# Performance work log

Measured on AMD Instinct MI355X. Metric: run time of the kernel, lower is better.

Reference implementation:

```python
import jax, jax.numpy as jnp
import numpy as np
import math

B, S, MEM, D, H = 2, 2048, 512, 1024, 16
DH = D // H  # 64


def setup_inputs() -> dict:
    key = jax.random.key(0)
    ks = jax.random.split(key, 12)
    s = 1.0 / math.sqrt(D)
    return {
        "x": jax.random.normal(ks[0], (B, S, D), jnp.float32),
        "mems": jax.random.normal(ks[1], (B, MEM, D), jnp.float32),
        "freqs_cis": jax.random.normal(ks[2], (S, 32), jnp.float32),
        "mask": jax.random.randint(ks[3], (B, MEM + S), 0, 2, jnp.int32),
        "Wq": jax.random.normal(ks[4], (D, D), jnp.float32) * s,
        "bq": jnp.zeros((D,), jnp.float32),
        "Wk": jax.random.normal(ks[5], (D, D), jnp.float32) * s,
        "bk": jnp.zeros((D,), jnp.float32),
        "Wv": jax.random.normal(ks[6], (D, D), jnp.float32) * s,
        "bv": jnp.zeros((D,), jnp.float32),
        "Wo": jax.random.normal(ks[7], (D, D), jnp.float32) * s,
        "bo": jnp.zeros((D,), jnp.float32),
    }


def _split_heads(t):
    # [B, T, D] -> [B, H, T, DH]
    b, t_, _ = t.shape
    return t.reshape(b, t_, H, DH).transpose(0, 2, 1, 3)


def reference(x, mems, freqs_cis, mask, Wq, bq, Wk, bk, Wv, bv, Wo, bo):
    # mems prepended along sequence for K/V (torch: c = cat([mems, x], 1))
    c = jnp.concatenate([mems, x], axis=1)  # [B, MEM+S, D]
    Q = _split_heads(x @ Wq.T + bq)          # [B, H, S, DH]
    K = _split_heads(c @ Wk.T + bk)          # [B, H, Skv, DH]
    V = _split_heads(c @ Wv.T + bv)          # [B, H, Skv, DH]

    scores = jnp.einsum("bhqd,bhkd->bhqk", Q, K) / math.sqrt(DH)
    m = mask.astype(jnp.float32)             # [B, Skv]
    scores = scores - 1e6 * (1.0 - m[:, None, None, :])
    attn = jax.nn.softmax(scores, axis=-1)   # dropout omitted (eval mode)
    out = jnp.einsum("bhqk,bhkd->bhqd", attn, V)  # [B, H, S, DH]
    out = out.transpose(0, 2, 1, 3).reshape(B, S, D)
    return out @ Wo.T + bo
```

## Files before the change

kernel.cpp:

```cpp
#include <hip/hip_runtime.h>
#include <math.h>

#define NB   2
#define SQ   2048
#define SMEM 512
#define SKVN 2560
#define ND   1024
#define NH   16
#define DHN  64
#define NBH  32

typedef unsigned short u16;
typedef short bf16x8 __attribute__((ext_vector_type(8)));
typedef float f32x4 __attribute__((ext_vector_type(4)));
typedef u16 u16x4 __attribute__((ext_vector_type(4)));
typedef u16 u16x8 __attribute__((ext_vector_type(8)));

#define CSC   0.1803368801111204f

__device__ __forceinline__ u16 f2bf(float f) {
    unsigned u = __float_as_uint(f);
    u += 0x7FFFu + ((u >> 16) & 1u);
    return (u16)(u >> 16);
}

__device__ __forceinline__ float bf2f(u16 v) {
    return __uint_as_float(((unsigned)v) << 16);
}

__device__ __forceinline__ void async16(u16* lds, const u16* g) {
    __builtin_amdgcn_global_load_lds(
        (const __attribute__((address_space(1))) void*)g,
        (__attribute__((address_space(3))) void*)lds, 16, 0, 0);
}

__device__ __forceinline__ unsigned lds_off(const void* p) {
    return (unsigned)(uintptr_t)(const __attribute__((address_space(3))) void*)p;
}

__device__ __forceinline__ u16x4 tr_read(unsigned a) {
    u16x4 d;
    asm volatile("ds_read_b64_tr_b16 %0, %1" : "=v"(d) : "v"(a) : "memory");
    return d;
}

__device__ __forceinline__ unsigned cvtpk(float lo, float hi) {
    unsigned r;
    asm("v_cvt_pk_bf16_f32 %0, %1, %2" : "=v"(r) : "v"(lo), "v"(hi));
    return r;
}

__device__ __forceinline__ float exp2r(float x) {
    float r;
    asm("v_exp_f32 %0, %1" : "=v"(r) : "v"(x));
    return r;
}

union PKU { unsigned u[2]; u16x4 v; };
union U8  { struct { u16x4 lo, hi; } p; bf16x8 v; };

__global__ __launch_bounds__(256)
void cvt_all(const float* __restrict__ x, const float* __restrict__ mems,
             const float* __restrict__ W0, const float* __restrict__ W1,
             const float* __restrict__ W2, const float* __restrict__ W3,
             u16* __restrict__ xb, u16* __restrict__ memb,
             u16* __restrict__ d0, u16* __restrict__ d1,
             u16* __restrict__ d2, u16* __restrict__ d3,
             const int* __restrict__ mask, u16* __restrict__ mb16)
{
    const int bid = blockIdx.x;
    if (bid >= 4608) {
        const int i = (bid - 4608) * 256 + threadIdx.x;
        if (i < NB * SKVN)
            mb16[i] = mask[i] ? (u16)0 : f2bf(1.0e6f * CSC);
        return;
    }
    size_t i = ((size_t)bid * 256 + threadIdx.x) * 8;
    const float* s; u16* d;
    if (i < 4194304) { s = x; d = xb; }
    else if (i < 5242880) { s = mems; d = memb; i -= 4194304; }
    else {
        size_t off = i - 5242880;
        const int wi = (int)(off >> 20);
        i = off & 1048575;
        switch (wi) {
            case 0:  s = W0; d = d0; break;
            case 1:  s = W1; d = d1; break;
            case 2:  s = W2; d = d2; break;
            default: s = W3; d = d3; break;
        }
    }
    float4 a = *(const float4*)(s + i);
    float4 b = *(const float4*)(s + i + 4);
    u16x8 o;
    o[0]=f2bf(a.x); o[1]=f2bf(a.y); o[2]=f2bf(a.z); o[3]=f2bf(a.w);
    o[4]=f2bf(b.x); o[5]=f2bf(b.y); o[6]=f2bf(b.z); o[7]=f2bf(b.w);
    *(u16x8*)(d + i) = o;
}

__device__ __forceinline__ const u16* arow_ptr(const u16* x, const u16* mems,
                                               int grow, int T, int memLen) {
    int b = grow >= T ? 1 : 0;
    int t = grow - b * T;
    if (memLen > 0 && t < memLen)
        return mems + ((size_t)(b * memLen + t)) * ND;
    return x + ((size_t)(b * (T - memLen) + (t - memLen))) * ND;
}

__device__ __forceinline__
void gemm64_body(const u16* __restrict__ x, const u16* __restrict__ mems,
                 const u16* __restrict__ W, const float* __restrict__ bias,
                 void* __restrict__ out, int T, int memLen, int mode,
                 int bx, int by, u16* As0, u16* As1, u16* Bs0, u16* Bs1)
{
    u16* As[2] = {As0, As1};
    u16* Bs[2] = {Bs0, Bs1};

    const int lane = threadIdx.x;
    const int lg = lane >> 4, li = lane & 15;
    const int row0 = bx * 64, col0 = by * 64;

    const int srow = lane >> 2;
    const int sslot = lane & 3;

    f32x4 acc[4][4];
    const f32x4 zf = {0.f, 0.f, 0.f, 0.f};
#pragma unroll
    for (int m = 0; m < 4; ++m)
#pragma unroll
        for (int n = 0; n < 4; ++n) acc[m][n] = zf;

    auto stage = [&](int c, int kt) {
        const int k0 = kt * 32;
#pragma unroll
        for (int ch = 0; ch < 4; ++ch) {
            const int r = ch * 16 + srow;
            const int gs = sslot ^ ((r ^ (r >> 2)) & 3);
            async16(&As[c][ch * 512],
                    arow_ptr(x, mems, row0 + r, T, memLen) + k0 + gs * 8);
        }
#pragma unroll
        for (int ch = 0; ch < 4; ++ch) {
            const int r = ch * 16 + srow;
            const int gs = sslot ^ ((r ^ (r >> 2)) & 3);
            async16(&Bs[c][ch * 512],
                    W + (size_t)(col0 + r) * ND + k0 + gs * 8);
        }
    };

    stage(0, 0);
    __builtin_amdgcn_sched_barrier(0);
    stage(1, 1);
    __builtin_amdgcn_sched_barrier(0);

    int cur = 0;
    for (int kt = 0; kt < 32; ++kt) {
        if (kt == 31) asm volatile("s_waitcnt vmcnt(0)" ::: "memory");
        else          asm volatile("s_waitcnt vmcnt(8)" ::: "memory");
        __builtin_amdgcn_sched_barrier(0);

        bf16x8 af[4], bfr[4];
#pragma unroll
        for (int m = 0; m < 4; ++m) {
            const int r = m * 16 + li;
            af[m] = *(const bf16x8*)&As[cur][r * 32 + ((lg ^ ((r ^ (r >> 2)) & 3)) << 3)];
        }
#pragma unroll
        for (int n = 0; n < 4; ++n) {
            const int r = n * 16 + li;
            bfr[n] = *(const bf16x8*)&Bs[cur][r * 32 + ((lg ^ ((r ^ (r >> 2)) & 3)) << 3)];
        }
        asm volatile("s_waitcnt lgkmcnt(0)" ::: "memory");
        __builtin_amdgcn_sched_barrier(0);
        if (kt + 2 < 32) stage(cur, kt + 2);

#pragma unroll
        for (int m = 0; m < 4; ++m)
#pragma unroll
            for (int n = 0; n < 4; ++n)
                acc[m][n] = __builtin_amdgcn_mfma_f32_16x16x32_bf16(
                                af[m], bfr[n], acc[m][n], 0, 0, 0);
        cur ^= 1;
    }

#pragma unroll
    for (int n = 0; n < 4; ++n) {
        const int col = col0 + n * 16 + li;
        const float bv = bias[col];
#pragma unroll
        for (int m = 0; m < 4; ++m) {
            const int rbase = row0 + m * 16 + 4 * lg;
            if (mode == 0) {
                float* o = (float*)out;
#pragma unroll
                for (int r = 0; r < 4; ++r)
                    o[(size_t)(rbase + r) * ND + col] = acc[m][n][r] + bv;
            } else if (mode == 1) {
                u16* o = (u16*)out;
                const int h = col >> 6, dh = col & 63;
#pragma unroll
                for (int r = 0; r < 4; ++r) {
                    const int grow = rbase + r;
                    const int b = grow >= T ? 1 : 0;
                    const int t = grow - b * T;
                    o[(((size_t)b * NH + h) * T + t) * DHN + dh] =
                        f2bf(acc[m][n][r] + bv);
                }
            } else {
                u16* o = (u16*)out;
                const int h = col >> 6, dh = col & 63;
                const int b = rbase >= T ? 1 : 0;
                const int t = rbase - b * T;
                u16x4 pk;
                pk[0] = f2bf(acc[m][n][0] + bv);
                pk[1] = f2bf(acc[m][n][1] + bv);
                pk[2] = f2bf(acc[m][n][2] + bv);
                pk[3] = f2bf(acc[m][n][3] + bv);
                *(u16x4*)&o[(((size_t)b * NH + h) * DHN + dh) * (size_t)T + t] = pk;
            }
        }
    }
}

__global__ __launch_bounds__(64)
void gemm_qkv(const u16* __restrict__ xb, const u16* __restrict__ memb,
              const u16* __restrict__ Wq, const float* __restrict__ bq, u16* Qb,
              const u16* __restrict__ Wk, const float* __restrict__ bk, u16* Kb,
              const u16* __restrict__ Wv, const float* __restrict__ bv, u16* Vtb)
{
    __shared__ u16 As[2][64 * 32];
    __shared__ u16 Bs[2][64 * 32];
    const int id = (blockIdx.x & 7) * 448 + (blockIdx.x >> 3);
    if (id < 1024) {
        gemm64_body(xb, nullptr, Wq, bq, Qb, SQ, 0, 1, id >> 4, id & 15,
                    As[0], As[1], Bs[0], Bs[1]);
    } else if (id < 2304) {
        const int t = id - 1024;
        gemm64_body(xb, memb, Wk, bk, Kb, SKVN, SMEM, 1, t >> 4, t & 15,
                    As[0], As[1], Bs[0], Bs[1]);
    } else {
        const int t = id - 2304;
        gemm64_body(xb, memb, Wv, bv, Vtb, SKVN, SMEM, 2, t >> 4, t & 15,
                    As[0], As[1], Bs[0], Bs[1]);
    }
}

__global__ __launch_bounds__(64)
void gemm_o(const u16* __restrict__ x, const u16* __restrict__ W,
            const float* __restrict__ bias, float* __restrict__ out)
{
    __shared__ u16 As[2][64 * 32];
    __shared__ u16 Bs[2][64 * 32];
    const int id = (blockIdx.x & 7) * 128 + (blockIdx.x >> 3);
    gemm64_body(x, nullptr, W, bias, out, SQ, 0, 0, id >> 4, id & 15,
                As[0], As[1], Bs[0], Bs[1]);
}

__global__ __launch_bounds__(512)
void attn_mfma(const u16* __restrict__ Qw, const u16* __restrict__ Kw,
               const u16* __restrict__ Vt, const u16* __restrict__ mb16,
               u16* __restrict__ AO)
{
    __shared__ u16 Ks[2][64 * 64];
    __shared__ u16 Vs[2][64 * 64];
    __shared__ u16 Ps[8][1024];
    __shared__ u16 Ms[SKVN];

    const int tid  = threadIdx.x;
    const int wave = tid >> 6, lane = tid & 63;
    const int lg = lane >> 4, li = lane & 15;

    const int wg = blockIdx.x;
    const int sw = (wg & 7) * 64 + (wg >> 3);
    const int bh = sw >> 4;
    const int q0 = (sw & 15) * 128;
    const int b = bh >> 4, h = bh & 15;

    const u16* Kg = Kw + (size_t)bh * SKVN * DHN;
    const u16* Vg = Vt + (size_t)bh * DHN * SKVN;
    const u16* m16row = mb16 + (size_t)b * SKVN;

    bf16x8 qA0, qA1;
    {
        const u16* Qp = Qw + ((size_t)bh * SQ + q0 + wave * 16 + li) * DHN;
        qA0 = *(const bf16x8*)(Qp + lg * 8);
        qA1 = *(const bf16x8*)(Qp + 32 + lg * 8);
    }

    for (int i = tid * 8; i < SKVN; i += 4096)
        *(u16x8*)&Ms[i] = *(const u16x8*)(m16row + i);

    U8 ou;
#pragma unroll
    for (int i = 0; i < 4; ++i) { ou.p.lo[i] = 0x3F80; ou.p.hi[i] = 0x3F80; }
    const bf16x8 onesb = ou.v;

    const int srow = lane >> 3, sslot = lane & 7;

    auto stage = [&](int c, int t) {
        const int kv0 = t * 64;
        const int r = wave * 8 + srow;
        async16(&Ks[c][wave * 512],
                Kg + (size_t)(kv0 + r) * DHN + ((sslot ^ (r & 7)) << 3));
        async16(&Vs[c][wave * 512],
                Vg + (size_t)r * SKVN + kv0 + ((sslot ^ (r & 7)) << 3));
    };

    f32x4 oA[4], laccA;
    const f32x4 zf = {0.f, 0.f, 0.f, 0.f};
#pragma unroll
    for (int n = 0; n < 4; ++n) oA[n] = zf;
    laccA = zf;

    u16* Pw = &Ps[wave][0];
    const unsigned paA = lds_off(Pw) + 256u * lg + 8u * li;

    __syncthreads();
    __builtin_amdgcn_sched_barrier(0);
    stage(0, 0);
    __builtin_amdgcn_sched_barrier(0);
    stage(1, 1);
    __builtin_amdgcn_sched_barrier(0);

    const int NT = SKVN / 64;
    int cur = 0;
    for (int t = 0; t < NT; ++t) {
        if (t == NT - 1) asm volatile("s_waitcnt vmcnt(0)" ::: "memory");
        else             asm volatile("s_waitcnt vmcnt(2)" ::: "memory");
        __builtin_amdgcn_s_barrier();
        __builtin_amdgcn_sched_barrier(0);

        float mbc[4];
#pragma unroll
        for (int n = 0; n < 4; ++n)
            mbc[n] = bf2f(Ms[t * 64 + n * 16 + li]);

        __builtin_amdgcn_s_setprio(1);
        f32x4 sA[4];
#pragma unroll
        for (int n = 0; n < 4; ++n) {
            const int r = n * 16 + li;
            bf16x8 kb0 = *(const bf16x8*)&Ks[cur][r * 64 + ((lg ^ (r & 7)) << 3)];
            bf16x8 kb1 = *(const bf16x8*)&Ks[cur][r * 64 + (((4 + lg) ^ (r & 7)) << 3)];
            f32x4 z = zf;
            z     = __builtin_amdgcn_mfma_f32_16x16x32_bf16(qA0, kb0, z, 0, 0, 0);
            sA[n] = __builtin_amdgcn_mfma_f32_16x16x32_bf16(qA1, kb1, z, 0, 0, 0);
        }
        __builtin_amdgcn_s_setprio(0);

#pragma unroll
        for (int n = 0; n < 4; ++n) {
            const float mb = mbc[n];
            const int pw = (n * 16 + li) * 16 + lg * 4;
            PKU ua;
            ua.u[0] = cvtpk(exp2r(fmaf(sA[n][0], CSC, -mb)),
                            exp2r(fmaf(sA[n][1], CSC, -mb)));
            ua.u[1] = cvtpk(exp2r(fmaf(sA[n][2], CSC, -mb)),
                            exp2r(fmaf(sA[n][3], CSC, -mb)));
            *(u16x4*)&Pw[pw] = ua.v;
        }

        u16x4 a00 = tr_read(paA);
        u16x4 a01 = tr_read(paA + 128);
        u16x4 a10 = tr_read(paA + 1024);
        u16x4 a11 = tr_read(paA + 1024 + 128);
        asm volatile("s_waitcnt lgkmcnt(0)" ::: "memory");
        __builtin_amdgcn_sched_barrier(0);
        U8 pA0, pA1;
        pA0.p.lo = a00; pA0.p.hi = a01;
        pA1.p.lo = a10; pA1.p.hi = a11;

        __builtin_amdgcn_s_setprio(1);
        laccA = __builtin_amdgcn_mfma_f32_16x16x32_bf16(pA0.v, onesb, laccA, 0, 0, 0);
        laccA = __builtin_amdgcn_mfma_f32_16x16x32_bf16(pA1.v, onesb, laccA, 0, 0, 0);
#pragma unroll
        for (int n = 0; n < 4; ++n) {
            const int r = n * 16 + li;
            bf16x8 vb0 = *(const bf16x8*)&Vs[cur][r * 64 + ((lg ^ (r & 7)) << 3)];
            bf16x8 vb1 = *(const bf16x8*)&Vs[cur][r * 64 + (((4 + lg) ^ (r & 7)) << 3)];
            oA[n] = __builtin_amdgcn_mfma_f32_16x16x32_bf16(pA0.v, vb0, oA[n], 0, 0, 0);
            oA[n] = __builtin_amdgcn_mfma_f32_16x16x32_bf16(pA1.v, vb1, oA[n], 0, 0, 0);
        }
        __builtin_amdgcn_s_setprio(0);

        asm volatile("s_waitcnt lgkmcnt(0)" ::: "memory");
        __builtin_amdgcn_s_barrier();
        __builtin_amdgcn_sched_barrier(0);

        if (t + 2 < NT) stage(cur, t + 2);
        cur ^= 1;
    }

#pragma unroll
    for (int r = 0; r < 4; ++r) {
        const float invA = 1.f / laccA[r];
        const int rowA = q0 + wave * 16 + 4 * lg + r;
#pragma unroll
        for (int n = 0; n < 4; ++n) {
            const int col = h * DHN + n * 16 + li;
            AO[((size_t)b * SQ + rowA) * ND + col] = f2bf(oA[n][r] * invA);
        }
    }
}

extern "C" void kernel_launch(void* const* d_in, const int* in_sizes, int n_in,
                              void* d_out, int out_size, void* d_ws, size_t ws_size,
                              hipStream_t stream)
{
    const float* x    = (const float*)d_in[0];
    const float* mems = (const float*)d_in[1];
    const int*   mask = (const int*)d_in[3];
    const float* Wq = (const float*)d_in[4];  const float* bq = (const float*)d_in[5];
    const float* Wk = (const float*)d_in[6];  const float* bk = (const float*)d_in[7];
    const float* Wv = (const float*)d_in[8];  const float* bv = (const float*)d_in[9];
    const float* Wo = (const float*)d_in[10]; const float* bo = (const float*)d_in[11];
    float* out = (float*)d_out;

    u16* ws = (u16*)d_ws;
    u16* xb   = ws;
    u16* memb = xb   + (size_t)NB * SQ * ND;
    u16* Wqb  = memb + (size_t)NB * SMEM * ND;
    u16* Wkb  = Wqb + (size_t)ND * ND;
    u16* Wvb  = Wkb + (size_t)ND * ND;
    u16* Wob  = Wvb + (size_t)ND * ND;
    u16* Qb   = Wob + (size_t)ND * ND;
    u16* Kb   = Qb  + (size_t)NB * NH * SQ * DHN;
    u16* Vtb  = Kb  + (size_t)NB * NH * SKVN * DHN;
    u16* AOb  = Vtb + (size_t)NB * NH * SKVN * DHN;
    u16* mb16 = AOb + (size_t)NB * SQ * ND;

    const dim3 blk(256);
    cvt_all<<<dim3(4628), blk, 0, stream>>>(x, mems, Wq, Wk, Wv, Wo,
                                            xb, memb, Wqb, Wkb, Wvb, Wob,
                                            mask, mb16);
    gemm_qkv<<<dim3(3584), dim3(64), 0, stream>>>(xb, memb,
                                                  Wqb, bq, Qb,
                                                  Wkb, bk, Kb,
                                                  Wvb, bv, Vtb);
    attn_mfma<<<dim3(512), dim3(512), 0, stream>>>(Qb, Kb, Vtb, mb16, AOb);
    gemm_o<<<dim3(1024), dim3(64), 0, stream>>>(AOb, Wob, bo, out);
}
```

Baseline: 150.1 us.

## Load GEMM operands directly from global into registers, drop LDS staging

Replaces the shared-memory double-buffered async staging in the 64x64 GEMM body with direct per-lane global loads of MFMA fragments, using an even/odd register ping-pong to prefetch the next k-step. This removes LDS traffic, swizzle math and waitcnt synchronisation, and frees shared memory. In exchange, global accesses become strided across rows and rely on cache for reuse, with less latency hiding than the previous async pipeline.

```diff
diff --git a/kernel.cpp b/kernel.cpp
--- a/kernel.cpp
+++ b/kernel.cpp
@@ -111,17 +111,20 @@
 void gemm64_body(const u16* __restrict__ x, const u16* __restrict__ mems,
                  const u16* __restrict__ W, const float* __restrict__ bias,
                  void* __restrict__ out, int T, int memLen, int mode,
-                 int bx, int by, u16* As0, u16* As1, u16* Bs0, u16* Bs1)
-{
-    u16* As[2] = {As0, As1};
-    u16* Bs[2] = {Bs0, Bs1};
-
+                 int bx, int by)
+{
     const int lane = threadIdx.x;
     const int lg = lane >> 4, li = lane & 15;
     const int row0 = bx * 64, col0 = by * 64;
 
-    const int srow = lane >> 2;
-    const int sslot = lane & 3;
+    const u16* Ar[4];
+    const u16* Br[4];
+#pragma unroll
+    for (int m = 0; m < 4; ++m)
+        Ar[m] = arow_ptr(x, mems, row0 + m * 16 + li, T, memLen) + lg * 8;
+#pragma unroll
+    for (int n = 0; n < 4; ++n)
+        Br[n] = W + (size_t)(col0 + n * 16 + li) * ND + lg * 8;
 
     f32x4 acc[4][4];
     const f32x4 zf = {0.f, 0.f, 0.f, 0.f};
@@ -130,57 +133,38 @@
 #pragma unroll
         for (int n = 0; n < 4; ++n) acc[m][n] = zf;
 
-    auto stage = [&](int c, int kt) {
-        const int k0 = kt * 32;
-#pragma unroll
-        for (int ch = 0; ch < 4; ++ch) {
-            const int r = ch * 16 + srow;
-            const int gs = sslot ^ ((r ^ (r >> 2)) & 3);
-            async16(&As[c][ch * 512],
-                    arow_ptr(x, mems, row0 + r, T, memLen) + k0 + gs * 8);
-        }
-#pragma unroll
-        for (int ch = 0; ch < 4; ++ch) {
-            const int r = ch * 16 + srow;
-            const int gs = sslot ^ ((r ^ (r >> 2)) & 3);
-            async16(&Bs[c][ch * 512],
-                    W + (size_t)(col0 + r) * ND + k0 + gs * 8);
-        }
-    };
-
-    stage(0, 0);
-    __builtin_amdgcn_sched_barrier(0);
-    stage(1, 1);
-    __builtin_amdgcn_sched_barrier(0);
-
-    int cur = 0;
-    for (int kt = 0; kt < 32; ++kt) {
-        if (kt == 31) asm volatile("s_waitcnt vmcnt(0)" ::: "memory");
-        else          asm volatile("s_waitcnt vmcnt(8)" ::: "memory");
-        __builtin_amdgcn_sched_barrier(0);
-
-        bf16x8 af[4], bfr[4];
+    bf16x8 aE[4], bE[4], aO[4], bO[4];
+#pragma unroll
+    for (int m = 0; m < 4; ++m) {
+        aE[m] = *(const bf16x8*)(Ar[m]);
+        bE[m] = *(const bf16x8*)(Br[m]);
+    }
+
+    for (int kt = 0; kt < 32; kt += 2) {
 #pragma unroll
         for (int m = 0; m < 4; ++m) {
-            const int r = m * 16 + li;
-            af[m] = *(const bf16x8*)&As[cur][r * 32 + ((lg ^ ((r ^ (r >> 2)) & 3)) << 3)];
-        }
-#pragma unroll
-        for (int n = 0; n < 4; ++n) {
-            const int r = n * 16 + li;
-            bfr[n] = *(const bf16x8*)&Bs[cur][r * 32 + ((lg ^ ((r ^ (r >> 2)) & 3)) << 3)];
-        }
-        asm volatile("s_waitcnt lgkmcnt(0)" ::: "memory");
-        __builtin_amdgcn_sched_barrier(0);
-        if (kt + 2 < 32) stage(cur, kt + 2);
-
+            aO[m] = *(const bf16x8*)(Ar[m] + (kt + 1) * 32);
+            bO[m] = *(const bf16x8*)(Br[m] + (kt + 1) * 32);
+        }
 #pragma unroll
         for (int m = 0; m < 4; ++m)
 #pragma unroll
             for (int n = 0; n < 4; ++n)
                 acc[m][n] = __builtin_amdgcn_mfma_f32_16x16x32_bf16(
-                                af[m], bfr[n], acc[m][n], 0, 0, 0);
-        cur ^= 1;
+                                aE[m], bE[n], acc[m][n], 0, 0, 0);
+        if (kt + 2 < 32) {
+#pragma unroll
+            for (int m = 0; m < 4; ++m) {
+                aE[m] = *(const bf16x8*)(Ar[m] + (kt + 2) * 32);
+                bE[m] = *(const bf16x8*)(Br[m] + (kt + 2) * 32);
+            }
+        }
+#pragma unroll
+        for (int m = 0; m < 4; ++m)
+#pragma unroll
+            for (int n = 0; n < 4; ++n)
+                acc[m][n] = __builtin_amdgcn_mfma_f32_16x16x32_bf16(
+                                aO[m], bO[n], acc[m][n], 0, 0, 0);
     }
 
 #pragma unroll
@@ -228,20 +212,15 @@
               const u16* __restrict__ Wk, const float* __restrict__ bk, u16* Kb,
               const u16* __restrict__ Wv, const float* __restrict__ bv, u16* Vtb)
 {
-    __shared__ u16 As[2][64 * 32];
-    __shared__ u16 Bs[2][64 * 32];
     const int id = (blockIdx.x & 7) * 448 + (blockIdx.x >> 3);
     if (id < 1024) {
-        gemm64_body(xb, nullptr, Wq, bq, Qb, SQ, 0, 1, id >> 4, id & 15,
-                    As[0], As[1], Bs[0], Bs[1]);
+        gemm64_body(xb, nullptr, Wq, bq, Qb, SQ, 0, 1, id >> 4, id & 15);
     } else if (id < 2304) {
         const int t = id - 1024;
-        gemm64_body(xb, memb, Wk, bk, Kb, SKVN, SMEM, 1, t >> 4, t & 15,
-                    As[0], As[1], Bs[0], Bs[1]);
+        gemm64_body(xb, memb, Wk, bk, Kb, SKVN, SMEM, 1, t >> 4, t & 15);
     } else {
         const int t = id - 2304;
-        gemm64_body(xb, memb, Wv, bv, Vtb, SKVN, SMEM, 2, t >> 4, t & 15,
-                    As[0], As[1], Bs[0], Bs[1]);
+        gemm64_body(xb, memb, Wv, bv, Vtb, SKVN, SMEM, 2, t >> 4, t & 15);
     }
 }
 
@@ -249,11 +228,8 @@
 void gemm_o(const u16* __restrict__ x, const u16* __restrict__ W,
             const float* __restrict__ bias, float* __restrict__ out)
 {
-    __shared__ u16 As[2][64 * 32];
-    __shared__ u16 Bs[2][64 * 32];
     const int id = (blockIdx.x & 7) * 128 + (blockIdx.x >> 3);
-    gemm64_body(x, nullptr, W, bias, out, SQ, 0, 0, id >> 4, id & 15,
-                As[0], As[1], Bs[0], Bs[1]);
+    gemm64_body(x, nullptr, W, bias, out, SQ, 0, 0, id >> 4, id & 15);
 }
 
 __global__ __launch_bounds__(512)
```

Measured after the change: 227.2 us. 51.4% more time.

## Split attention over KV halves and add combine kernel

Applied to the files above, without the earlier changes.

Attention workgroups now each process half of the key/value sequence, doubling the grid to improve CU occupancy and load balance. Each half writes unnormalized bf16 partial outputs and row sums to workspace, and a new combine kernel sums the two halves and normalizes. This adds an extra kernel launch, extra global memory traffic for partials, and a slight precision loss from rounding partials to bf16.

```diff
diff --git a/kernel.cpp b/kernel.cpp
--- a/kernel.cpp
+++ b/kernel.cpp
@@ -259,7 +259,7 @@
 __global__ __launch_bounds__(512)
 void attn_mfma(const u16* __restrict__ Qw, const u16* __restrict__ Kw,
                const u16* __restrict__ Vt, const u16* __restrict__ mb16,
-               u16* __restrict__ AO)
+               u16* __restrict__ PO, float* __restrict__ Lb)
 {
     __shared__ u16 Ks[2][64 * 64];
     __shared__ u16 Vs[2][64 * 64];
@@ -271,14 +271,15 @@
     const int lg = lane >> 4, li = lane & 15;
 
     const int wg = blockIdx.x;
-    const int sw = (wg & 7) * 64 + (wg >> 3);
-    const int bh = sw >> 4;
-    const int q0 = (sw & 15) * 128;
-    const int b = bh >> 4, h = bh & 15;
+    const int sw = (wg & 7) * 128 + (wg >> 3);
+    const int bh   = sw >> 5;
+    const int q0   = ((sw >> 1) & 15) * 128;
+    const int half = sw & 1;
+    const int t0 = half * 20, t1 = t0 + 20;
 
     const u16* Kg = Kw + (size_t)bh * SKVN * DHN;
     const u16* Vg = Vt + (size_t)bh * DHN * SKVN;
-    const u16* m16row = mb16 + (size_t)b * SKVN;
+    const u16* m16row = mb16 + (size_t)(bh >> 4) * SKVN;
 
     bf16x8 qA0, qA1;
     {
@@ -317,15 +318,14 @@
 
     __syncthreads();
     __builtin_amdgcn_sched_barrier(0);
-    stage(0, 0);
+    stage(0, t0);
     __builtin_amdgcn_sched_barrier(0);
-    stage(1, 1);
+    stage(1, t0 + 1);
     __builtin_amdgcn_sched_barrier(0);
 
-    const int NT = SKVN / 64;
     int cur = 0;
-    for (int t = 0; t < NT; ++t) {
-        if (t == NT - 1) asm volatile("s_waitcnt vmcnt(0)" ::: "memory");
+    for (int t = t0; t < t1; ++t) {
+        if (t == t1 - 1) asm volatile("s_waitcnt vmcnt(0)" ::: "memory");
         else             asm volatile("s_waitcnt vmcnt(2)" ::: "memory");
         __builtin_amdgcn_s_barrier();
         __builtin_amdgcn_sched_barrier(0);
@@ -387,20 +387,46 @@
         __builtin_amdgcn_s_barrier();
         __builtin_amdgcn_sched_barrier(0);
 
-        if (t + 2 < NT) stage(cur, t + 2);
+        if (t + 2 < t1) stage(cur, t + 2);
         cur ^= 1;
     }
 
+    u16* POh = PO + (size_t)half * NBH * SQ * DHN;
+    float* Lh = Lb + (size_t)half * NBH * SQ;
 #pragma unroll
     for (int r = 0; r < 4; ++r) {
-        const float invA = 1.f / laccA[r];
         const int rowA = q0 + wave * 16 + 4 * lg + r;
 #pragma unroll
         for (int n = 0; n < 4; ++n) {
-            const int col = h * DHN + n * 16 + li;
-            AO[((size_t)b * SQ + rowA) * ND + col] = f2bf(oA[n][r] * invA);
-        }
-    }
+            const int c = n * 16 + li;
+            POh[((size_t)bh * SQ + rowA) * DHN + c] = f2bf(oA[n][r]);
+        }
+        if (li == 0) Lh[(size_t)bh * SQ + rowA] = laccA[r];
+    }
+}
+
+__global__ __launch_bounds__(256)
+void attn_combine(const u16* __restrict__ PO, const float* __restrict__ Lb,
+                  u16* __restrict__ AO)
+{
+    const size_t idx = ((size_t)blockIdx.x * 256 + threadIdx.x) * 8;
+    const int row = (int)(idx >> 10);
+    const int col = (int)(idx & 1023);
+    const int b = row >> 11, q = row & 2047;
+    const int h = col >> 6, dh = col & 63;
+    const int bh = b * NH + h;
+    const size_t pbase = ((size_t)bh * SQ + q) * DHN + dh;
+    const size_t hs = (size_t)NBH * SQ * DHN;
+
+    u16x8 pa = *(const u16x8*)&PO[pbase];
+    u16x8 pb = *(const u16x8*)&PO[hs + pbase];
+    const float l = Lb[(size_t)bh * SQ + q] + Lb[(size_t)NBH * SQ + bh * SQ + q];
+    const float inv = 1.f / l;
+    u16x8 o;
+#pragma unroll
+    for (int i = 0; i < 8; ++i)
+        o[i] = f2bf((bf2f(pa[i]) + bf2f(pb[i])) * inv);
+    *(u16x8*)&AO[idx] = o;
 }
 
 extern "C" void kernel_launch(void* const* d_in, const int* in_sizes, int n_in,
@@ -428,6 +454,8 @@
     u16* Vtb  = Kb  + (size_t)NB * NH * SKVN * DHN;
     u16* AOb  = Vtb + (size_t)NB * NH * SKVN * DHN;
     u16* mb16 = AOb + (size_t)NB * SQ * ND;
+    u16* POb  = mb16 + (size_t)NB * SKVN;
+    float* Lbf = (float*)(POb + (size_t)2 * NBH * SQ * DHN);
 
     const dim3 blk(256);
     cvt_all<<<dim3(4628), blk, 0, stream>>>(x, mems, Wq, Wk, Wv, Wo,
@@ -437,6 +465,7 @@
                                                   Wqb, bq, Qb,
                                                   Wkb, bk, Kb,
                                                   Wvb, bv, Vtb);
-    attn_mfma<<<dim3(512), dim3(512), 0, stream>>>(Qb, Kb, Vtb, mb16, AOb);
+    attn_mfma<<<dim3(1024), dim3(512), 0, stream>>>(Qb, Kb, Vtb, mb16, POb, Lbf);
+    attn_combine<<<dim3(2048), blk, 0, stream>>>(POb, Lbf, AOb);
     gemm_o<<<dim3(1024), dim3(64), 0, stream>>>(AOb, Wob, bo, out);
 }
```

Measured after the change: 158.2 us. 5.4% more time.
